# Kernel tuning notes

Hardware: AMD Instinct MI355X
Metric: run time of the kernel (lower is better)

## Reference

```python
import jax, jax.numpy as jnp
import numpy as np


def setup_inputs() -> dict:
    key = jax.random.key(0)
    ks = jax.random.split(key, 9)
    C_in, C_out, D = 64, 64, 24
    B, H, W = 4, 96, 96
    s_in = 1.0 / np.sqrt(C_in)
    s_d = 1.0 / np.sqrt(D)
    return {
        "x": jax.random.normal(ks[0], (B, C_in, H, W), dtype=jnp.float32),
        "wq": jax.random.uniform(ks[1], (D, C_in), jnp.float32, -s_in, s_in),
        "bq": jax.random.uniform(ks[2], (D,), jnp.float32, -s_in, s_in),
        "wk": jax.random.uniform(ks[3], (D, C_in), jnp.float32, -s_in, s_in),
        "bk": jax.random.uniform(ks[4], (D,), jnp.float32, -s_in, s_in),
        "wv": jax.random.uniform(ks[5], (D, C_in), jnp.float32, -s_in, s_in),
        "bv": jax.random.uniform(ks[6], (D,), jnp.float32, -s_in, s_in),
        "wo": jax.random.uniform(ks[7], (C_out, D), jnp.float32, -s_d, s_d),
        "bo": jax.random.uniform(ks[8], (C_out,), jnp.float32, -s_d, s_d),
    }


def reference(x, wq, bq, wk, bk, wv, bv, wo, bo):
    B, C, H, W = x.shape
    D = wq.shape[0]
    xf = x.reshape(B, C, H * W)  # [B, C, N]
    # 1x1 convs == channel-wise linear projections
    q = jnp.einsum('dc,bcn->bdn', wq, xf) + bq[None, :, None]  # [B, D, N]
    k = jnp.einsum('dc,bcn->bdn', wk, xf) + bk[None, :, None]
    v = jnp.einsum('dc,bcn->bdn', wv, xf) + bv[None, :, None]
    scale = 1.0 / jnp.sqrt(jnp.asarray(D, x.dtype))
    scores = jnp.einsum('bdi,bdj->bij', q, k) * scale  # [B, N, N]
    weights = jax.nn.softmax(scores, axis=-1)
    # attn_out[b,d,i] = sum_j v[b,d,j] * weights[b,i,j]
    attn = jnp.einsum('bdj,bij->bdi', v, weights)  # [B, D, N]
    out = jnp.einsum('od,bdn->bon', wo, attn) + bo[None, :, None]
    return out.reshape(B, -1, H, W)
```

## Files before the change

kernel.cpp:

```cpp
#include <hip/hip_runtime.h>
#include <stdint.h>

#define NPIX 9216
#define CIN 64
#define DD 24
#define DP 32
#define JQ 1152
#define NIT 18

typedef __attribute__((ext_vector_type(8))) short short8;
typedef __attribute__((ext_vector_type(4))) float f32x4;
typedef __attribute__((ext_vector_type(4))) unsigned int u32x4;

__device__ __forceinline__ unsigned short f2bf(float f) {
    unsigned int u = __builtin_bit_cast(unsigned int, f);
    u += 0x7fffu + ((u >> 16) & 1u);
    return (unsigned short)(u >> 16);
}
__device__ __forceinline__ unsigned int pkbf(float lo, float hi) {
    unsigned int r;
    asm("v_cvt_pk_bf16_f32 %0, %1, %2" : "=v"(r) : "v"(lo), "v"(hi));
    return r;
}

__global__ __launch_bounds__(256) void qkv_proj_kernel(
    const float* __restrict__ x,
    const float* __restrict__ wq, const float* __restrict__ bq,
    const float* __restrict__ wk, const float* __restrict__ bk,
    const float* __restrict__ wv, const float* __restrict__ bv,
    unsigned short* __restrict__ qr, unsigned short* __restrict__ kr,
    unsigned short* __restrict__ vdn)
{
    const int p = blockIdx.y;
    const int tid = blockIdx.x * 256 + threadIdx.x;
    const int b = tid / NPIX;
    const int n = tid - b * NPIX;
    const float* xb = x + (size_t)b * CIN * NPIX + n;
    float xv[CIN];
#pragma unroll
    for (int c = 0; c < CIN; ++c) xv[c] = xb[(size_t)c * NPIX];

    const float* wm = (p == 0) ? wq : (p == 1) ? wk : wv;
    const float* bm = (p == 0) ? bq : (p == 1) ? bk : bv;

    float acc[DD];
#pragma unroll
    for (int d = 0; d < DD; ++d) acc[d] = bm[d];
#pragma unroll 4
    for (int c = 0; c < CIN; ++c) {
        const float xc = xv[c];
#pragma unroll
        for (int d = 0; d < DD; ++d) acc[d] = fmaf(wm[d * CIN + c], xc, acc[d]);
    }

    if (p == 2) {
        const size_t vbase = (size_t)b * DD * NPIX + n;
#pragma unroll
        for (int d = 0; d < DD; ++d) vdn[vbase + (size_t)d * NPIX] = f2bf(acc[d]);
    } else {
        alignas(16) unsigned short row[DP];
        const float sc = (p == 0) ? (float)(0.20412414523193154 * 1.4426950408889634) : 1.0f;
#pragma unroll
        for (int d = 0; d < DD; ++d) row[d] = f2bf(acc[d] * sc);
#pragma unroll
        for (int d = DD; d < DP; ++d) row[d] = 0;
        unsigned short* dst = ((p == 0) ? qr : kr) + (size_t)(b * NPIX + n) * DP;
        const u32x4* r4 = (const u32x4*)row;
#pragma unroll
        for (int i = 0; i < 4; ++i) ((u32x4*)dst)[i] = r4[i];
    }
}

__global__ __launch_bounds__(512) void attn_kernel(
    const unsigned short* __restrict__ qr,
    const unsigned short* __restrict__ kr,
    const unsigned short* __restrict__ vdn,
    float* __restrict__ part)
{
    __shared__ __align__(16) unsigned char pool[20480 + 18432];
    unsigned short* kpool = (unsigned short*)pool;
    unsigned short* vpool = (unsigned short*)(pool + 20480);

    const int tile = blockIdx.x, jh = blockIdx.y, b = blockIdx.z;
    const int t = threadIdx.x;
    const int w = t >> 6, lane = t & 63;
    const int g = lane >> 4, c = lane & 15;
    const int sq = w >> 2;
    const int p  = w & 3;

    for (int i = t; i < 4 * 8 * 72; i += 512) {
        const int q_ = i / 576, rem = i - q_ * 576;
        const int r_ = rem / 72, col = rem - r_ * 72;
        vpool[q_ * 2304 + (24 + r_) * 72 + col] = (r_ == 0) ? (unsigned short)0x3F80 : 0;
    }

    const int qbaseA = tile * 64 + sq * 32 + c;
    const short8 qfA = *(const short8*)(qr + ((size_t)(b * NPIX + qbaseA)) * DP + g * 8);
    const short8 qfB = *(const short8*)(qr + ((size_t)(b * NPIX + qbaseA + 16)) * DP + g * 8);

    const unsigned short* kb = kr + (size_t)b * NPIX * DP;
    const unsigned short* vb = vdn + (size_t)b * DD * NPIX;
    const int jbase = jh * 4608;

    const int khw = t & 1, kq = t >> 7, kjn = (t >> 1) & 63;
    const int kR = ((kjn >> 5) & 1) * 32 + ((kjn >> 2) & 1) * 16
                 + ((kjn >> 4) & 1) * 8 + ((kjn >> 3) & 1) * 4 + (kjn & 3);
    unsigned short* kdst = kpool + kq * 2560 + kR * 40 + khw * 16;
    const unsigned short* ksrc0 = kb + ((size_t)(jbase + kq * JQ + kjn)) * DP + khw * 16;

    const int vq = t / 96, vrem = t - vq * 96, vd = vrem >> 2, vpt = t & 3;
    unsigned short* vdst = vpool + vq * 2304 + vd * 72 + vpt * 16;
    const unsigned short* vsrc0 = vb + (size_t)vd * NPIX + jbase + vq * JQ + vpt * 16;

    const unsigned short* kT = kpool + p * 2560;
    const unsigned short* vT = vpool + p * 2304;

    f32x4 aA0 = {0.f, 0.f, 0.f, 0.f};
    f32x4 aA1 = {0.f, 0.f, 0.f, 0.f};
    f32x4 aB0 = {0.f, 0.f, 0.f, 0.f};
    f32x4 aB1 = {0.f, 0.f, 0.f, 0.f};
    const f32x4 zf = {0.f, 0.f, 0.f, 0.f};

    u32x4 pk0, pk1, pv0, pv1;
    {
        const u32x4* sk = (const u32x4*)ksrc0;
        pk0 = sk[0]; pk1 = sk[1];
        if (t < 384) { const u32x4* sv = (const u32x4*)vsrc0; pv0 = sv[0]; pv1 = sv[1]; }
    }

    for (int it = 0; it < NIT; ++it) {
        __syncthreads();
        *(u32x4*)kdst = pk0; *(u32x4*)(kdst + 8) = pk1;
        if (t < 384) { *(u32x4*)vdst = pv0; *(u32x4*)(vdst + 8) = pv1; }
        __syncthreads();

        if (it + 1 < NIT) {
            const int jn = (it + 1) * 64;
            const u32x4* sk = (const u32x4*)(ksrc0 + (size_t)jn * DP);
            pk0 = sk[0]; pk1 = sk[1];
            if (t < 384) { const u32x4* sv = (const u32x4*)(vsrc0 + jn); pv0 = sv[0]; pv1 = sv[1]; }
        }

        const short8 kf0 = *(const short8*)(kT + ( 0 + c) * 40 + g * 8);
        const short8 kf1 = *(const short8*)(kT + (16 + c) * 40 + g * 8);
        const short8 kf2 = *(const short8*)(kT + (32 + c) * 40 + g * 8);
        const short8 kf3 = *(const short8*)(kT + (48 + c) * 40 + g * 8);
        __builtin_amdgcn_s_setprio(1);
        f32x4 sA0 = __builtin_amdgcn_mfma_f32_16x16x32_bf16(kf0, qfA, zf, 0, 0, 0);
        f32x4 sA1 = __builtin_amdgcn_mfma_f32_16x16x32_bf16(kf1, qfA, zf, 0, 0, 0);
        f32x4 sA2 = __builtin_amdgcn_mfma_f32_16x16x32_bf16(kf2, qfA, zf, 0, 0, 0);
        f32x4 sA3 = __builtin_amdgcn_mfma_f32_16x16x32_bf16(kf3, qfA, zf, 0, 0, 0);
        f32x4 sB0 = __builtin_amdgcn_mfma_f32_16x16x32_bf16(kf0, qfB, zf, 0, 0, 0);
        f32x4 sB1 = __builtin_amdgcn_mfma_f32_16x16x32_bf16(kf1, qfB, zf, 0, 0, 0);
        f32x4 sB2 = __builtin_amdgcn_mfma_f32_16x16x32_bf16(kf2, qfB, zf, 0, 0, 0);
        f32x4 sB3 = __builtin_amdgcn_mfma_f32_16x16x32_bf16(kf3, qfB, zf, 0, 0, 0);
        __builtin_amdgcn_s_setprio(0);

        union { short8 s8; unsigned int u32[4]; } fa0, fa1, fb0, fb1;
        {
            float p0[4], p1[4], p2[4], p3[4];
#pragma unroll
            for (int r = 0; r < 4; ++r) {
                p0[r] = __builtin_amdgcn_exp2f(sA0[r]);
                p1[r] = __builtin_amdgcn_exp2f(sA1[r]);
                p2[r] = __builtin_amdgcn_exp2f(sA2[r]);
                p3[r] = __builtin_amdgcn_exp2f(sA3[r]);
            }
            fa0.u32[0] = pkbf(p0[0], p0[1]); fa0.u32[1] = pkbf(p0[2], p0[3]);
            fa0.u32[2] = pkbf(p1[0], p1[1]); fa0.u32[3] = pkbf(p1[2], p1[3]);
            fa1.u32[0] = pkbf(p2[0], p2[1]); fa1.u32[1] = pkbf(p2[2], p2[3]);
            fa1.u32[2] = pkbf(p3[0], p3[1]); fa1.u32[3] = pkbf(p3[2], p3[3]);
        }
        {
            float p0[4], p1[4], p2[4], p3[4];
#pragma unroll
            for (int r = 0; r < 4; ++r) {
                p0[r] = __builtin_amdgcn_exp2f(sB0[r]);
                p1[r] = __builtin_amdgcn_exp2f(sB1[r]);
                p2[r] = __builtin_amdgcn_exp2f(sB2[r]);
                p3[r] = __builtin_amdgcn_exp2f(sB3[r]);
            }
            fb0.u32[0] = pkbf(p0[0], p0[1]); fb0.u32[1] = pkbf(p0[2], p0[3]);
            fb0.u32[2] = pkbf(p1[0], p1[1]); fb0.u32[3] = pkbf(p1[2], p1[3]);
            fb1.u32[0] = pkbf(p2[0], p2[1]); fb1.u32[1] = pkbf(p2[2], p2[3]);
            fb1.u32[2] = pkbf(p3[0], p3[1]); fb1.u32[3] = pkbf(p3[2], p3[3]);
        }

        const short8 vl0 = *(const short8*)(vT + (c)      * 72 +      g * 8);
        const short8 vh0 = *(const short8*)(vT + (16 + c) * 72 +      g * 8);
        const short8 vl1 = *(const short8*)(vT + (c)      * 72 + 32 + g * 8);
        const short8 vh1 = *(const short8*)(vT + (16 + c) * 72 + 32 + g * 8);
        __builtin_amdgcn_s_setprio(1);
        aA0 = __builtin_amdgcn_mfma_f32_16x16x32_bf16(vl0, fa0.s8, aA0, 0, 0, 0);
        aA1 = __builtin_amdgcn_mfma_f32_16x16x32_bf16(vh0, fa0.s8, aA1, 0, 0, 0);
        aA0 = __builtin_amdgcn_mfma_f32_16x16x32_bf16(vl1, fa1.s8, aA0, 0, 0, 0);
        aA1 = __builtin_amdgcn_mfma_f32_16x16x32_bf16(vh1, fa1.s8, aA1, 0, 0, 0);
        aB0 = __builtin_amdgcn_mfma_f32_16x16x32_bf16(vl0, fb0.s8, aB0, 0, 0, 0);
        aB1 = __builtin_amdgcn_mfma_f32_16x16x32_bf16(vh0, fb0.s8, aB1, 0, 0, 0);
        aB0 = __builtin_amdgcn_mfma_f32_16x16x32_bf16(vl1, fb1.s8, aB0, 0, 0, 0);
        aB1 = __builtin_amdgcn_mfma_f32_16x16x32_bf16(vh1, fb1.s8, aB1, 0, 0, 0);
        __builtin_amdgcn_s_setprio(0);
    }
    __syncthreads();

    float* om = (float*)pool;
    *(f32x4*)(om + (w * 32 + c) * 36 + 4 * g) = aA0;
    *(f32x4*)(om + (w * 32 + c) * 36 + 16 + 4 * g) = aA1;
    *(f32x4*)(om + (w * 32 + 16 + c) * 36 + 4 * g) = aB0;
    *(f32x4*)(om + (w * 32 + 16 + c) * 36 + 16 + 4 * g) = aB1;
    __syncthreads();

    const int q = t & 63, og = t >> 6;
    const int sqe = q >> 5, qc = q & 31;
    const float* o0 = om + ((sqe * 4 + 0) * 32 + qc) * 36;
    const float* o1 = om + ((sqe * 4 + 1) * 32 + qc) * 36;
    const float* o2 = om + ((sqe * 4 + 2) * 32 + qc) * 36;
    const float* o3 = om + ((sqe * 4 + 3) * 32 + qc) * 36;
    float* dst = part + ((size_t)((b * 2 + jh) * NPIX + tile * 64 + q)) * 26;
#pragma unroll
    for (int i = 0; i < 3; ++i) {
        const int d = og * 3 + i;
        dst[d] = o0[d] + o1[d] + o2[d] + o3[d];
    }
    if (og == 7) dst[24] = o0[24] + o1[24] + o2[24] + o3[24];
}

__global__ __launch_bounds__(256) void combine_kernel(
    const float* __restrict__ part,
    const float* __restrict__ wo, const float* __restrict__ bo,
    float* __restrict__ out)
{
    __shared__ float od_lds[64][25];
    __shared__ float wo_lds[64 * DD];
    __shared__ float bo_lds[64];
    const int tile = blockIdx.x, b = blockIdx.y;
    const int t = threadIdx.x;
    for (int i = t; i < 64 * DD; i += 256) wo_lds[i] = wo[i];
    if (t < 64) bo_lds[t] = bo[t];

    const int q = t & 63, c2 = t >> 6;
    {
        const float* pA = part + ((size_t)((b * 2 + 0) * NPIX + tile * 64 + q)) * 26;
        const float* pB = part + ((size_t)((b * 2 + 1) * NPIX + tile * 64 + q)) * 26;
#pragma unroll
        for (int k = 0; k < 7; ++k) {
            const int i = c2 * 7 + k;
            if (i < 25) od_lds[q][i] = pA[i] + pB[i];
        }
    }
    __syncthreads();

    const float inv = 1.0f / od_lds[q][24];
    float od[DD];
#pragma unroll
    for (int d = 0; d < DD; ++d) od[d] = od_lds[q][d] * inv;

    const int n_g = tile * 64 + q;
#pragma unroll
    for (int oo = 0; oo < 16; ++oo) {
        const int o = c2 * 16 + oo;
        float a = bo_lds[o];
#pragma unroll
        for (int d = 0; d < DD; ++d) a = fmaf(wo_lds[o * DD + d], od[d], a);
        out[((size_t)(b * 64 + o)) * NPIX + n_g] = a;
    }
}

extern "C" void kernel_launch(void* const* d_in, const int* in_sizes, int n_in,
                              void* d_out, int out_size, void* d_ws, size_t ws_size,
                              hipStream_t stream) {
    const float* x  = (const float*)d_in[0];
    const float* wq = (const float*)d_in[1];
    const float* bq = (const float*)d_in[2];
    const float* wk = (const float*)d_in[3];
    const float* bk = (const float*)d_in[4];
    const float* wv = (const float*)d_in[5];
    const float* bv = (const float*)d_in[6];
    const float* wo = (const float*)d_in[7];
    const float* bo = (const float*)d_in[8];
    float* out = (float*)d_out;

    unsigned short* qr  = (unsigned short*)d_ws;
    unsigned short* kr  = qr + (size_t)4 * NPIX * DP;
    unsigned short* vdn = kr + (size_t)4 * NPIX * DP;
    float* part = (float*)((char*)d_ws + 6488064);
    hipLaunchKernelGGL(qkv_proj_kernel, dim3(4 * NPIX / 256, 3), dim3(256), 0, stream,
                       x, wq, bq, wk, bk, wv, bv, qr, kr, vdn);
    hipLaunchKernelGGL(attn_kernel, dim3(NPIX / 64, 2, 4), dim3(512), 0, stream,
                       qr, kr, vdn, part);
    hipLaunchKernelGGL(combine_kernel, dim3(NPIX / 64, 4), dim3(256), 0, stream,
                       part, wo, bo, out);
}
```

Baseline: 97.32 us.

## Halve attention block to 4 waves, each covering all 64 queries

The attention kernel moves from 8 waves (two query halves times four key quarters) to 4 waves, where each wave handles all 64 queries for its key quarter. K/V fragments loaded from LDS are now reused across four query groups instead of two, which cuts LDS reads per unit of MFMA work. The global-to-LDS staging is redistributed across 256 threads. In exchange, each wave holds twice the accumulators and score registers, which may lower occupancy, and there are fewer waves per block to hide latency.

```diff
diff --git a/kernel.cpp b/kernel.cpp
--- a/kernel.cpp
+++ b/kernel.cpp
@@ -71,7 +71,7 @@
     }
 }
 
-__global__ __launch_bounds__(512) void attn_kernel(
+__global__ __launch_bounds__(256) void attn_kernel(
     const unsigned short* __restrict__ qr,
     const unsigned short* __restrict__ kr,
     const unsigned short* __restrict__ vdn,
@@ -85,144 +85,216 @@
     const int t = threadIdx.x;
     const int w = t >> 6, lane = t & 63;
     const int g = lane >> 4, c = lane & 15;
-    const int sq = w >> 2;
-    const int p  = w & 3;
-
-    for (int i = t; i < 4 * 8 * 72; i += 512) {
+    const int p = w;
+
+    for (int i = t; i < 4 * 8 * 72; i += 256) {
         const int q_ = i / 576, rem = i - q_ * 576;
         const int r_ = rem / 72, col = rem - r_ * 72;
         vpool[q_ * 2304 + (24 + r_) * 72 + col] = (r_ == 0) ? (unsigned short)0x3F80 : 0;
     }
 
-    const int qbaseA = tile * 64 + sq * 32 + c;
-    const short8 qfA = *(const short8*)(qr + ((size_t)(b * NPIX + qbaseA)) * DP + g * 8);
-    const short8 qfB = *(const short8*)(qr + ((size_t)(b * NPIX + qbaseA + 16)) * DP + g * 8);
+    const int qbase = tile * 64 + c;
+    const unsigned short* qp = qr + (size_t)b * NPIX * DP;
+    const short8 qfA = *(const short8*)(qp + (size_t)(qbase +  0) * DP + g * 8);
+    const short8 qfB = *(const short8*)(qp + (size_t)(qbase + 16) * DP + g * 8);
+    const short8 qfC = *(const short8*)(qp + (size_t)(qbase + 32) * DP + g * 8);
+    const short8 qfD = *(const short8*)(qp + (size_t)(qbase + 48) * DP + g * 8);
 
     const unsigned short* kb = kr + (size_t)b * NPIX * DP;
     const unsigned short* vb = vdn + (size_t)b * DD * NPIX;
     const int jbase = jh * 4608;
 
-    const int khw = t & 1, kq = t >> 7, kjn = (t >> 1) & 63;
+    const int kjn = (t >> 1) & 63, khw = t & 1, kqa = t >> 7;
     const int kR = ((kjn >> 5) & 1) * 32 + ((kjn >> 2) & 1) * 16
                  + ((kjn >> 4) & 1) * 8 + ((kjn >> 3) & 1) * 4 + (kjn & 3);
-    unsigned short* kdst = kpool + kq * 2560 + kR * 40 + khw * 16;
-    const unsigned short* ksrc0 = kb + ((size_t)(jbase + kq * JQ + kjn)) * DP + khw * 16;
-
-    const int vq = t / 96, vrem = t - vq * 96, vd = vrem >> 2, vpt = t & 3;
-    unsigned short* vdst = vpool + vq * 2304 + vd * 72 + vpt * 16;
-    const unsigned short* vsrc0 = vb + (size_t)vd * NPIX + jbase + vq * JQ + vpt * 16;
+    unsigned short* kdst0 = kpool + kqa * 2560 + kR * 40 + khw * 16;
+    unsigned short* kdst1 = kdst0 + 2 * 2560;
+    const unsigned short* ksrcA = kb + ((size_t)(jbase + kqa * JQ + kjn)) * DP + khw * 16;
+    const unsigned short* ksrcB = ksrcA + (size_t)2 * JQ * DP;
+
+    const int g0 = t, g1 = t + 256, g2 = t + 512;
+    const int vq0 = g0 / 192, vr0 = g0 - vq0 * 192, vd0 = vr0 >> 3, vp0 = vr0 & 7;
+    const int vq1 = g1 / 192, vr1 = g1 - vq1 * 192, vd1 = vr1 >> 3, vp1 = vr1 & 7;
+    const int vq2 = g2 / 192, vr2 = g2 - vq2 * 192, vd2 = vr2 >> 3, vp2 = vr2 & 7;
+    unsigned short* vdst0 = vpool + vq0 * 2304 + vd0 * 72 + vp0 * 8;
+    unsigned short* vdst1 = vpool + vq1 * 2304 + vd1 * 72 + vp1 * 8;
+    unsigned short* vdst2 = vpool + vq2 * 2304 + vd2 * 72 + vp2 * 8;
+    const unsigned short* vsrcA = vb + (size_t)vd0 * NPIX + jbase + vq0 * JQ + vp0 * 8;
+    const unsigned short* vsrcB = vb + (size_t)vd1 * NPIX + jbase + vq1 * JQ + vp1 * 8;
+    const unsigned short* vsrcC = vb + (size_t)vd2 * NPIX + jbase + vq2 * JQ + vp2 * 8;
 
     const unsigned short* kT = kpool + p * 2560;
     const unsigned short* vT = vpool + p * 2304;
 
-    f32x4 aA0 = {0.f, 0.f, 0.f, 0.f};
-    f32x4 aA1 = {0.f, 0.f, 0.f, 0.f};
-    f32x4 aB0 = {0.f, 0.f, 0.f, 0.f};
-    f32x4 aB1 = {0.f, 0.f, 0.f, 0.f};
+    f32x4 aA0 = {0.f,0.f,0.f,0.f}, aA1 = aA0;
+    f32x4 aB0 = aA0, aB1 = aA0;
+    f32x4 aC0 = aA0, aC1 = aA0;
+    f32x4 aD0 = aA0, aD1 = aA0;
     const f32x4 zf = {0.f, 0.f, 0.f, 0.f};
 
-    u32x4 pk0, pk1, pv0, pv1;
+    u32x4 pk0a, pk0b, pk1a, pk1b, pv0, pv1, pv2;
     {
-        const u32x4* sk = (const u32x4*)ksrc0;
-        pk0 = sk[0]; pk1 = sk[1];
-        if (t < 384) { const u32x4* sv = (const u32x4*)vsrc0; pv0 = sv[0]; pv1 = sv[1]; }
+        const u32x4* s0 = (const u32x4*)ksrcA; pk0a = s0[0]; pk0b = s0[1];
+        const u32x4* s1 = (const u32x4*)ksrcB; pk1a = s1[0]; pk1b = s1[1];
+        pv0 = *(const u32x4*)vsrcA; pv1 = *(const u32x4*)vsrcB; pv2 = *(const u32x4*)vsrcC;
     }
 
     for (int it = 0; it < NIT; ++it) {
         __syncthreads();
-        *(u32x4*)kdst = pk0; *(u32x4*)(kdst + 8) = pk1;
-        if (t < 384) { *(u32x4*)vdst = pv0; *(u32x4*)(vdst + 8) = pv1; }
+        *(u32x4*)kdst0 = pk0a; *(u32x4*)(kdst0 + 8) = pk0b;
+        *(u32x4*)kdst1 = pk1a; *(u32x4*)(kdst1 + 8) = pk1b;
+        *(u32x4*)vdst0 = pv0; *(u32x4*)vdst1 = pv1; *(u32x4*)vdst2 = pv2;
         __syncthreads();
 
         if (it + 1 < NIT) {
             const int jn = (it + 1) * 64;
-            const u32x4* sk = (const u32x4*)(ksrc0 + (size_t)jn * DP);
-            pk0 = sk[0]; pk1 = sk[1];
-            if (t < 384) { const u32x4* sv = (const u32x4*)(vsrc0 + jn); pv0 = sv[0]; pv1 = sv[1]; }
+            const u32x4* s0 = (const u32x4*)(ksrcA + (size_t)jn * DP); pk0a = s0[0]; pk0b = s0[1];
+            const u32x4* s1 = (const u32x4*)(ksrcB + (size_t)jn * DP); pk1a = s1[0]; pk1b = s1[1];
+            pv0 = *(const u32x4*)(vsrcA + jn);
+            pv1 = *(const u32x4*)(vsrcB + jn);
+            pv2 = *(const u32x4*)(vsrcC + jn);
         }
 
         const short8 kf0 = *(const short8*)(kT + ( 0 + c) * 40 + g * 8);
         const short8 kf1 = *(const short8*)(kT + (16 + c) * 40 + g * 8);
         const short8 kf2 = *(const short8*)(kT + (32 + c) * 40 + g * 8);
         const short8 kf3 = *(const short8*)(kT + (48 + c) * 40 + g * 8);
-        __builtin_amdgcn_s_setprio(1);
-        f32x4 sA0 = __builtin_amdgcn_mfma_f32_16x16x32_bf16(kf0, qfA, zf, 0, 0, 0);
-        f32x4 sA1 = __builtin_amdgcn_mfma_f32_16x16x32_bf16(kf1, qfA, zf, 0, 0, 0);
-        f32x4 sA2 = __builtin_amdgcn_mfma_f32_16x16x32_bf16(kf2, qfA, zf, 0, 0, 0);
-        f32x4 sA3 = __builtin_amdgcn_mfma_f32_16x16x32_bf16(kf3, qfA, zf, 0, 0, 0);
-        f32x4 sB0 = __builtin_amdgcn_mfma_f32_16x16x32_bf16(kf0, qfB, zf, 0, 0, 0);
-        f32x4 sB1 = __builtin_amdgcn_mfma_f32_16x16x32_bf16(kf1, qfB, zf, 0, 0, 0);
-        f32x4 sB2 = __builtin_amdgcn_mfma_f32_16x16x32_bf16(kf2, qfB, zf, 0, 0, 0);
-        f32x4 sB3 = __builtin_amdgcn_mfma_f32_16x16x32_bf16(kf3, qfB, zf, 0, 0, 0);
-        __builtin_amdgcn_s_setprio(0);
-
-        union { short8 s8; unsigned int u32[4]; } fa0, fa1, fb0, fb1;
-        {
-            float p0[4], p1[4], p2[4], p3[4];
-#pragma unroll
-            for (int r = 0; r < 4; ++r) {
-                p0[r] = __builtin_amdgcn_exp2f(sA0[r]);
-                p1[r] = __builtin_amdgcn_exp2f(sA1[r]);
-                p2[r] = __builtin_amdgcn_exp2f(sA2[r]);
-                p3[r] = __builtin_amdgcn_exp2f(sA3[r]);
-            }
-            fa0.u32[0] = pkbf(p0[0], p0[1]); fa0.u32[1] = pkbf(p0[2], p0[3]);
-            fa0.u32[2] = pkbf(p1[0], p1[1]); fa0.u32[3] = pkbf(p1[2], p1[3]);
-            fa1.u32[0] = pkbf(p2[0], p2[1]); fa1.u32[1] = pkbf(p2[2], p2[3]);
-            fa1.u32[2] = pkbf(p3[0], p3[1]); fa1.u32[3] = pkbf(p3[2], p3[3]);
-        }
-        {
-            float p0[4], p1[4], p2[4], p3[4];
-#pragma unroll
-            for (int r = 0; r < 4; ++r) {
-                p0[r] = __builtin_amdgcn_exp2f(sB0[r]);
-                p1[r] = __builtin_amdgcn_exp2f(sB1[r]);
-                p2[r] = __builtin_amdgcn_exp2f(sB2[r]);
-                p3[r] = __builtin_amdgcn_exp2f(sB3[r]);
-            }
-            fb0.u32[0] = pkbf(p0[0], p0[1]); fb0.u32[1] = pkbf(p0[2], p0[3]);
-            fb0.u32[2] = pkbf(p1[0], p1[1]); fb0.u32[3] = pkbf(p1[2], p1[3]);
-            fb1.u32[0] = pkbf(p2[0], p2[1]); fb1.u32[1] = pkbf(p2[2], p2[3]);
-            fb1.u32[2] = pkbf(p3[0], p3[1]); fb1.u32[3] = pkbf(p3[2], p3[3]);
-        }
-
         const short8 vl0 = *(const short8*)(vT + (c)      * 72 +      g * 8);
         const short8 vh0 = *(const short8*)(vT + (16 + c) * 72 +      g * 8);
         const short8 vl1 = *(const short8*)(vT + (c)      * 72 + 32 + g * 8);
         const short8 vh1 = *(const short8*)(vT + (16 + c) * 72 + 32 + g * 8);
-        __builtin_amdgcn_s_setprio(1);
-        aA0 = __builtin_amdgcn_mfma_f32_16x16x32_bf16(vl0, fa0.s8, aA0, 0, 0, 0);
-        aA1 = __builtin_amdgcn_mfma_f32_16x16x32_bf16(vh0, fa0.s8, aA1, 0, 0, 0);
-        aA0 = __builtin_amdgcn_mfma_f32_16x16x32_bf16(vl1, fa1.s8, aA0, 0, 0, 0);
-        aA1 = __builtin_amdgcn_mfma_f32_16x16x32_bf16(vh1, fa1.s8, aA1, 0, 0, 0);
-        aB0 = __builtin_amdgcn_mfma_f32_16x16x32_bf16(vl0, fb0.s8, aB0, 0, 0, 0);
-        aB1 = __builtin_amdgcn_mfma_f32_16x16x32_bf16(vh0, fb0.s8, aB1, 0, 0, 0);
-        aB0 = __builtin_amdgcn_mfma_f32_16x16x32_bf16(vl1, fb1.s8, aB0, 0, 0, 0);
-        aB1 = __builtin_amdgcn_mfma_f32_16x16x32_bf16(vh1, fb1.s8, aB1, 0, 0, 0);
-        __builtin_amdgcn_s_setprio(0);
+
+        {
+            __builtin_amdgcn_s_setprio(1);
+            f32x4 sA0 = __builtin_amdgcn_mfma_f32_16x16x32_bf16(kf0, qfA, zf, 0, 0, 0);
+            f32x4 sA1 = __builtin_amdgcn_mfma_f32_16x16x32_bf16(kf1, qfA, zf, 0, 0, 0);
+            f32x4 sA2 = __builtin_amdgcn_mfma_f32_16x16x32_bf16(kf2, qfA, zf, 0, 0, 0);
+            f32x4 sA3 = __builtin_amdgcn_mfma_f32_16x16x32_bf16(kf3, qfA, zf, 0, 0, 0);
+            f32x4 sB0 = __builtin_amdgcn_mfma_f32_16x16x32_bf16(kf0, qfB, zf, 0, 0, 0);
+            f32x4 sB1 = __builtin_amdgcn_mfma_f32_16x16x32_bf16(kf1, qfB, zf, 0, 0, 0);
+            f32x4 sB2 = __builtin_amdgcn_mfma_f32_16x16x32_bf16(kf2, qfB, zf, 0, 0, 0);
+            f32x4 sB3 = __builtin_amdgcn_mfma_f32_16x16x32_bf16(kf3, qfB, zf, 0, 0, 0);
+            __builtin_amdgcn_s_setprio(0);
+
+            union { short8 s8; unsigned int u32[4]; } fa0, fa1, fb0, fb1;
+            {
+                float p0[4], p1[4], p2[4], p3[4];
+#pragma unroll
+                for (int r = 0; r < 4; ++r) {
+                    p0[r] = __builtin_amdgcn_exp2f(sA0[r]);
+                    p1[r] = __builtin_amdgcn_exp2f(sA1[r]);
+                    p2[r] = __builtin_amdgcn_exp2f(sA2[r]);
+                    p3[r] = __builtin_amdgcn_exp2f(sA3[r]);
+                }
+                fa0.u32[0] = pkbf(p0[0], p0[1]); fa0.u32[1] = pkbf(p0[2], p0[3]);
+                fa0.u32[2] = pkbf(p1[0], p1[1]); fa0.u32[3] = pkbf(p1[2], p1[3]);
+                fa1.u32[0] = pkbf(p2[0], p2[1]); fa1.u32[1] = pkbf(p2[2], p2[3]);
+                fa1.u32[2] = pkbf(p3[0], p3[1]); fa1.u32[3] = pkbf(p3[2], p3[3]);
+            }
+            {
+                float p0[4], p1[4], p2[4], p3[4];
+#pragma unroll
+                for (int r = 0; r < 4; ++r) {
+                    p0[r] = __builtin_amdgcn_exp2f(sB0[r]);
+                    p1[r] = __builtin_amdgcn_exp2f(sB1[r]);
+                    p2[r] = __builtin_amdgcn_exp2f(sB2[r]);
+                    p3[r] = __builtin_amdgcn_exp2f(sB3[r]);
+                }
+                fb0.u32[0] = pkbf(p0[0], p0[1]); fb0.u32[1] = pkbf(p0[2], p0[3]);
+                fb0.u32[2] = pkbf(p1[0], p1[1]); fb0.u32[3] = pkbf(p1[2], p1[3]);
+                fb1.u32[0] = pkbf(p2[0], p2[1]); fb1.u32[1] = pkbf(p2[2], p2[3]);
+                fb1.u32[2] = pkbf(p3[0], p3[1]); fb1.u32[3] = pkbf(p3[2], p3[3]);
+            }
+
+            __builtin_amdgcn_s_setprio(1);
+            aA0 = __builtin_amdgcn_mfma_f32_16x16x32_bf16(vl0, fa0.s8, aA0, 0, 0, 0);
+            aA1 = __builtin_amdgcn_mfma_f32_16x16x32_bf16(vh0, fa0.s8, aA1, 0, 0, 0);
+            aA0 = __builtin_amdgcn_mfma_f32_16x16x32_bf16(vl1, fa1.s8, aA0, 0, 0, 0);
+            aA1 = __builtin_amdgcn_mfma_f32_16x16x32_bf16(vh1, fa1.s8, aA1, 0, 0, 0);
+            aB0 = __builtin_amdgcn_mfma_f32_16x16x32_bf16(vl0, fb0.s8, aB0, 0, 0, 0);
+            aB1 = __builtin_amdgcn_mfma_f32_16x16x32_bf16(vh0, fb0.s8, aB1, 0, 0, 0);
+            aB0 = __builtin_amdgcn_mfma_f32_16x16x32_bf16(vl1, fb1.s8, aB0, 0, 0, 0);
+            aB1 = __builtin_amdgcn_mfma_f32_16x16x32_bf16(vh1, fb1.s8, aB1, 0, 0, 0);
+            __builtin_amdgcn_s_setprio(0);
+        }
+        {
+            __builtin_amdgcn_s_setprio(1);
+            f32x4 sC0 = __builtin_amdgcn_mfma_f32_16x16x32_bf16(kf0, qfC, zf, 0, 0, 0);
+            f32x4 sC1 = __builtin_amdgcn_mfma_f32_16x16x32_bf16(kf1, qfC, zf, 0, 0, 0);
+            f32x4 sC2 = __builtin_amdgcn_mfma_f32_16x16x32_bf16(kf2, qfC, zf, 0, 0, 0);
+            f32x4 sC3 = __builtin_amdgcn_mfma_f32_16x16x32_bf16(kf3, qfC, zf, 0, 0, 0);
+            f32x4 sD0 = __builtin_amdgcn_mfma_f32_16x16x32_bf16(kf0, qfD, zf, 0, 0, 0);
+            f32x4 sD1 = __builtin_amdgcn_mfma_f32_16x16x32_bf16(kf1, qfD, zf, 0, 0, 0);
+            f32x4 sD2 = __builtin_amdgcn_mfma_f32_16x16x32_bf16(kf2, qfD, zf, 0, 0, 0);
+            f32x4 sD3 = __builtin_amdgcn_mfma_f32_16x16x32_bf16(kf3, qfD, zf, 0, 0, 0);
+            __builtin_amdgcn_s_setprio(0);
+
+            union { short8 s8; unsigned int u32[4]; } fc0, fc1, fd0, fd1;
+            {
+                float p0[4], p1[4], p2[4], p3[4];
+#pragma unroll
+                for (int r = 0; r < 4; ++r) {
+                    p0[r] = __builtin_amdgcn_exp2f(sC0[r]);
+                    p1[r] = __builtin_amdgcn_exp2f(sC1[r]);
+                    p2[r] = __builtin_amdgcn_exp2f(sC2[r]);
+                    p3[r] = __builtin_amdgcn_exp2f(sC3[r]);
+                }
+                fc0.u32[0] = pkbf(p0[0], p0[1]); fc0.u32[1] = pkbf(p0[2], p0[3]);
+                fc0.u32[2] = pkbf(p1[0], p1[1]); fc0.u32[3] = pkbf(p1[2], p1[3]);
+                fc1.u32[0] = pkbf(p2[0], p2[1]); fc1.u32[1] = pkbf(p2[2], p2[3]);
+                fc1.u32[2] = pkbf(p3[0], p3[1]); fc1.u32[3] = pkbf(p3[2], p3[3]);
+            }
+            {
+                float p0[4], p1[4], p2[4], p3[4];
+#pragma unroll
+                for (int r = 0; r < 4; ++r) {
+                    p0[r] = __builtin_amdgcn_exp2f(sD0[r]);
+                    p1[r] = __builtin_amdgcn_exp2f(sD1[r]);
+                    p2[r] = __builtin_amdgcn_exp2f(sD2[r]);
+                    p3[r] = __builtin_amdgcn_exp2f(sD3[r]);
+                }
+                fd0.u32[0] = pkbf(p0[0], p0[1]); fd0.u32[1] = pkbf(p0[2], p0[3]);
+                fd0.u32[2] = pkbf(p1[0], p1[1]); fd0.u32[3] = pkbf(p1[2], p1[3]);
+                fd1.u32[0] = pkbf(p2[0], p2[1]); fd1.u32[1] = pkbf(p2[2], p2[3]);
+                fd1.u32[2] = pkbf(p3[0], p3[1]); fd1.u32[3] = pkbf(p3[2], p3[3]);
+            }
+
+            __builtin_amdgcn_s_setprio(1);
+            aC0 = __builtin_amdgcn_mfma_f32_16x16x32_bf16(vl0, fc0.s8, aC0, 0, 0, 0);
+            aC1 = __builtin_amdgcn_mfma_f32_16x16x32_bf16(vh0, fc0.s8, aC1, 0, 0, 0);
+            aC0 = __builtin_amdgcn_mfma_f32_16x16x32_bf16(vl1, fc1.s8, aC0, 0, 0, 0);
+            aC1 = __builtin_amdgcn_mfma_f32_16x16x32_bf16(vh1, fc1.s8, aC1, 0, 0, 0);
+            aD0 = __builtin_amdgcn_mfma_f32_16x16x32_bf16(vl0, fd0.s8, aD0, 0, 0, 0);
+            aD1 = __builtin_amdgcn_mfma_f32_16x16x32_bf16(vh0, fd0.s8, aD1, 0, 0, 0);
+            aD0 = __builtin_amdgcn_mfma_f32_16x16x32_bf16(vl1, fd1.s8, aD0, 0, 0, 0);
+            aD1 = __builtin_amdgcn_mfma_f32_16x16x32_bf16(vh1, fd1.s8, aD1, 0, 0, 0);
+            __builtin_amdgcn_s_setprio(0);
+        }
     }
     __syncthreads();
 
     float* om = (float*)pool;
-    *(f32x4*)(om + (w * 32 + c) * 36 + 4 * g) = aA0;
-    *(f32x4*)(om + (w * 32 + c) * 36 + 16 + 4 * g) = aA1;
-    *(f32x4*)(om + (w * 32 + 16 + c) * 36 + 4 * g) = aB0;
-    *(f32x4*)(om + (w * 32 + 16 + c) * 36 + 16 + 4 * g) = aB1;
+    *(f32x4*)(om + (p * 64 + c)      * 36 + 4 * g) = aA0;
+    *(f32x4*)(om + (p * 64 + c)      * 36 + 16 + 4 * g) = aA1;
+    *(f32x4*)(om + (p * 64 + 16 + c) * 36 + 4 * g) = aB0;
+    *(f32x4*)(om + (p * 64 + 16 + c) * 36 + 16 + 4 * g) = aB1;
+    *(f32x4*)(om + (p * 64 + 32 + c) * 36 + 4 * g) = aC0;
+    *(f32x4*)(om + (p * 64 + 32 + c) * 36 + 16 + 4 * g) = aC1;
+    *(f32x4*)(om + (p * 64 + 48 + c) * 36 + 4 * g) = aD0;
+    *(f32x4*)(om + (p * 64 + 48 + c) * 36 + 16 + 4 * g) = aD1;
     __syncthreads();
 
     const int q = t & 63, og = t >> 6;
-    const int sqe = q >> 5, qc = q & 31;
-    const float* o0 = om + ((sqe * 4 + 0) * 32 + qc) * 36;
-    const float* o1 = om + ((sqe * 4 + 1) * 32 + qc) * 36;
-    const float* o2 = om + ((sqe * 4 + 2) * 32 + qc) * 36;
-    const float* o3 = om + ((sqe * 4 + 3) * 32 + qc) * 36;
+    const float* o0 = om + (0 * 64 + q) * 36;
+    const float* o1 = om + (1 * 64 + q) * 36;
+    const float* o2 = om + (2 * 64 + q) * 36;
+    const float* o3 = om + (3 * 64 + q) * 36;
     float* dst = part + ((size_t)((b * 2 + jh) * NPIX + tile * 64 + q)) * 26;
 #pragma unroll
-    for (int i = 0; i < 3; ++i) {
-        const int d = og * 3 + i;
-        dst[d] = o0[d] + o1[d] + o2[d] + o3[d];
-    }
-    if (og == 7) dst[24] = o0[24] + o1[24] + o2[24] + o3[24];
+    for (int k = 0; k < 7; ++k) {
+        const int i = og * 7 + k;
+        if (i < 25) dst[i] = (o0[i] + o1[i]) + (o2[i] + o3[i]);
+    }
 }
 
 __global__ __launch_bounds__(256) void combine_kernel(
@@ -284,9 +356,10 @@
     unsigned short* kr  = qr + (size_t)4 * NPIX * DP;
     unsigned short* vdn = kr + (size_t)4 * NPIX * DP;
     float* part = (float*)((char*)d_ws + 6488064);
+
     hipLaunchKernelGGL(qkv_proj_kernel, dim3(4 * NPIX / 256, 3), dim3(256), 0, stream,
                        x, wq, bq, wk, bk, wv, bv, qr, kr, vdn);
-    hipLaunchKernelGGL(attn_kernel, dim3(NPIX / 64, 2, 4), dim3(512), 0, stream,
+    hipLaunchKernelGGL(attn_kernel, dim3(NPIX / 64, 2, 4), dim3(256), 0, stream,
                        qr, kr, vdn, part);
     hipLaunchKernelGGL(combine_kernel, dim3(NPIX / 64, 4), dim3(256), 0, stream,
                        part, wo, bo, out);
```

Measured after the change: 117.8 us. 21.0% more time.

## Load K/V MFMA fragments directly from global memory, dropping LDS staging and barriers

Applied to the files above, without the earlier changes.

The attention kernel no longer stages K and V tiles through shared memory with two barriers per iteration. Each wave now reads its MFMA fragments straight from global memory (L2/L1-resident), prefetching K one iteration ahead. V is padded to 32 rows in the projection kernel, with the ones-row for the softmax denominator written there instead of in LDS, and the workspace offset is moved to fit it. This removes LDS traffic and sync stalls, but adds redundant global loads per wave and less coalesced V access.

```diff
diff --git a/kernel.cpp b/kernel.cpp
--- a/kernel.cpp
+++ b/kernel.cpp
@@ -54,9 +54,12 @@
     }
 
     if (p == 2) {
-        const size_t vbase = (size_t)b * DD * NPIX + n;
+        const size_t vbase = (size_t)b * DP * NPIX + n;
 #pragma unroll
         for (int d = 0; d < DD; ++d) vdn[vbase + (size_t)d * NPIX] = f2bf(acc[d]);
+        vdn[vbase + (size_t)24 * NPIX] = (unsigned short)0x3F80;
+#pragma unroll
+        for (int d = 25; d < DP; ++d) vdn[vbase + (size_t)d * NPIX] = 0;
     } else {
         alignas(16) unsigned short row[DP];
         const float sc = (p == 0) ? (float)(0.20412414523193154 * 1.4426950408889634) : 1.0f;
@@ -77,9 +80,7 @@
     const unsigned short* __restrict__ vdn,
     float* __restrict__ part)
 {
-    __shared__ __align__(16) unsigned char pool[20480 + 18432];
-    unsigned short* kpool = (unsigned short*)pool;
-    unsigned short* vpool = (unsigned short*)(pool + 20480);
+    __shared__ float om[8 * 32 * 36];
 
     const int tile = blockIdx.x, jh = blockIdx.y, b = blockIdx.z;
     const int t = threadIdx.x;
@@ -88,63 +89,44 @@
     const int sq = w >> 2;
     const int p  = w & 3;
 
-    for (int i = t; i < 4 * 8 * 72; i += 512) {
-        const int q_ = i / 576, rem = i - q_ * 576;
-        const int r_ = rem / 72, col = rem - r_ * 72;
-        vpool[q_ * 2304 + (24 + r_) * 72 + col] = (r_ == 0) ? (unsigned short)0x3F80 : 0;
-    }
-
-    const int qbaseA = tile * 64 + sq * 32 + c;
-    const short8 qfA = *(const short8*)(qr + ((size_t)(b * NPIX + qbaseA)) * DP + g * 8);
-    const short8 qfB = *(const short8*)(qr + ((size_t)(b * NPIX + qbaseA + 16)) * DP + g * 8);
+    const int qbase = tile * 64 + sq * 32 + c;
+    const unsigned short* qp = qr + (size_t)b * NPIX * DP;
+    const short8 qfA = *(const short8*)(qp + (size_t)(qbase +  0) * DP + g * 8);
+    const short8 qfB = *(const short8*)(qp + (size_t)(qbase + 16) * DP + g * 8);
 
     const unsigned short* kb = kr + (size_t)b * NPIX * DP;
-    const unsigned short* vb = vdn + (size_t)b * DD * NPIX;
-    const int jbase = jh * 4608;
-
-    const int khw = t & 1, kq = t >> 7, kjn = (t >> 1) & 63;
-    const int kR = ((kjn >> 5) & 1) * 32 + ((kjn >> 2) & 1) * 16
-                 + ((kjn >> 4) & 1) * 8 + ((kjn >> 3) & 1) * 4 + (kjn & 3);
-    unsigned short* kdst = kpool + kq * 2560 + kR * 40 + khw * 16;
-    const unsigned short* ksrc0 = kb + ((size_t)(jbase + kq * JQ + kjn)) * DP + khw * 16;
-
-    const int vq = t / 96, vrem = t - vq * 96, vd = vrem >> 2, vpt = t & 3;
-    unsigned short* vdst = vpool + vq * 2304 + vd * 72 + vpt * 16;
-    const unsigned short* vsrc0 = vb + (size_t)vd * NPIX + jbase + vq * JQ + vpt * 16;
-
-    const unsigned short* kT = kpool + p * 2560;
-    const unsigned short* vT = vpool + p * 2304;
-
-    f32x4 aA0 = {0.f, 0.f, 0.f, 0.f};
-    f32x4 aA1 = {0.f, 0.f, 0.f, 0.f};
-    f32x4 aB0 = {0.f, 0.f, 0.f, 0.f};
-    f32x4 aB1 = {0.f, 0.f, 0.f, 0.f};
+    const unsigned short* vb = vdn + (size_t)b * DP * NPIX;
+    const int jbase = jh * 4608 + p * JQ;
+
+    const int jinv0 = ((c >> 3) & 1) * 16 + ((c >> 2) & 1) * 8 + (c & 3);
+    const unsigned short* kp = kb + ((size_t)(jbase + jinv0)) * DP + g * 8;
+    const unsigned short* vpl = vb + (size_t)c * NPIX + jbase + g * 8;
+    const unsigned short* vph = vpl + (size_t)16 * NPIX;
+
+    f32x4 aA0 = {0.f,0.f,0.f,0.f}, aA1 = aA0;
+    f32x4 aB0 = aA0, aB1 = aA0;
     const f32x4 zf = {0.f, 0.f, 0.f, 0.f};
 
-    u32x4 pk0, pk1, pv0, pv1;
-    {
-        const u32x4* sk = (const u32x4*)ksrc0;
-        pk0 = sk[0]; pk1 = sk[1];
-        if (t < 384) { const u32x4* sv = (const u32x4*)vsrc0; pv0 = sv[0]; pv1 = sv[1]; }
-    }
+    short8 nk0 = *(const short8*)(kp);
+    short8 nk1 = *(const short8*)(kp + 128);
+    short8 nk2 = *(const short8*)(kp + 1024);
+    short8 nk3 = *(const short8*)(kp + 1152);
 
     for (int it = 0; it < NIT; ++it) {
-        __syncthreads();
-        *(u32x4*)kdst = pk0; *(u32x4*)(kdst + 8) = pk1;
-        if (t < 384) { *(u32x4*)vdst = pv0; *(u32x4*)(vdst + 8) = pv1; }
-        __syncthreads();
-
+        const short8 kf0 = nk0, kf1 = nk1, kf2 = nk2, kf3 = nk3;
+        const short8 vl0 = *(const short8*)(vpl);
+        const short8 vh0 = *(const short8*)(vph);
+        const short8 vl1 = *(const short8*)(vpl + 32);
+        const short8 vh1 = *(const short8*)(vph + 32);
+        vpl += 64; vph += 64;
         if (it + 1 < NIT) {
-            const int jn = (it + 1) * 64;
-            const u32x4* sk = (const u32x4*)(ksrc0 + (size_t)jn * DP);
-            pk0 = sk[0]; pk1 = sk[1];
-            if (t < 384) { const u32x4* sv = (const u32x4*)(vsrc0 + jn); pv0 = sv[0]; pv1 = sv[1]; }
-        }
-
-        const short8 kf0 = *(const short8*)(kT + ( 0 + c) * 40 + g * 8);
-        const short8 kf1 = *(const short8*)(kT + (16 + c) * 40 + g * 8);
-        const short8 kf2 = *(const short8*)(kT + (32 + c) * 40 + g * 8);
-        const short8 kf3 = *(const short8*)(kT + (48 + c) * 40 + g * 8);
+            kp += 2048;
+            nk0 = *(const short8*)(kp);
+            nk1 = *(const short8*)(kp + 128);
+            nk2 = *(const short8*)(kp + 1024);
+            nk3 = *(const short8*)(kp + 1152);
+        }
+
         __builtin_amdgcn_s_setprio(1);
         f32x4 sA0 = __builtin_amdgcn_mfma_f32_16x16x32_bf16(kf0, qfA, zf, 0, 0, 0);
         f32x4 sA1 = __builtin_amdgcn_mfma_f32_16x16x32_bf16(kf1, qfA, zf, 0, 0, 0);
@@ -186,10 +168,6 @@
             fb1.u32[2] = pkbf(p3[0], p3[1]); fb1.u32[3] = pkbf(p3[2], p3[3]);
         }
 
-        const short8 vl0 = *(const short8*)(vT + (c)      * 72 +      g * 8);
-        const short8 vh0 = *(const short8*)(vT + (16 + c) * 72 +      g * 8);
-        const short8 vl1 = *(const short8*)(vT + (c)      * 72 + 32 + g * 8);
-        const short8 vh1 = *(const short8*)(vT + (16 + c) * 72 + 32 + g * 8);
         __builtin_amdgcn_s_setprio(1);
         aA0 = __builtin_amdgcn_mfma_f32_16x16x32_bf16(vl0, fa0.s8, aA0, 0, 0, 0);
         aA1 = __builtin_amdgcn_mfma_f32_16x16x32_bf16(vh0, fa0.s8, aA1, 0, 0, 0);
@@ -201,9 +179,7 @@
         aB1 = __builtin_amdgcn_mfma_f32_16x16x32_bf16(vh1, fb1.s8, aB1, 0, 0, 0);
         __builtin_amdgcn_s_setprio(0);
     }
-    __syncthreads();
-
-    float* om = (float*)pool;
+
     *(f32x4*)(om + (w * 32 + c) * 36 + 4 * g) = aA0;
     *(f32x4*)(om + (w * 32 + c) * 36 + 16 + 4 * g) = aA1;
     *(f32x4*)(om + (w * 32 + 16 + c) * 36 + 4 * g) = aB0;
@@ -220,9 +196,9 @@
 #pragma unroll
     for (int i = 0; i < 3; ++i) {
         const int d = og * 3 + i;
-        dst[d] = o0[d] + o1[d] + o2[d] + o3[d];
-    }
-    if (og == 7) dst[24] = o0[24] + o1[24] + o2[24] + o3[24];
+        dst[d] = (o0[d] + o1[d]) + (o2[d] + o3[d]);
+    }
+    if (og == 7) dst[24] = (o0[24] + o1[24]) + (o2[24] + o3[24]);
 }
 
 __global__ __launch_bounds__(256) void combine_kernel(
@@ -283,7 +259,7 @@
     unsigned short* qr  = (unsigned short*)d_ws;
     unsigned short* kr  = qr + (size_t)4 * NPIX * DP;
     unsigned short* vdn = kr + (size_t)4 * NPIX * DP;
-    float* part = (float*)((char*)d_ws + 6488064);
+    float* part = (float*)((char*)d_ws + 7077888);
     hipLaunchKernelGGL(qkv_proj_kernel, dim3(4 * NPIX / 256, 3), dim3(256), 0, stream,
                        x, wq, bq, wk, bk, wv, bv, qr, kr, vdn);
     hipLaunchKernelGGL(attn_kernel, dim3(NPIX / 64, 2, 4), dim3(512), 0, stream,
```

New measurement: 159.2 us. 63.6% more time.
